# Kernel optimization log

Hardware: AMD Instinct MI355X
Metric: run time of the kernel (lower is better)

## Reference

```python
import jax, jax.numpy as jnp
import numpy as np

N_NODES = 100000
N_EDGES = 800000
HID = 128
EDIM = 32


def _mlp2(x, W1, b1, W2, b2):
    return jax.nn.relu(x @ W1 + b1) @ W2 + b2


def _edge_conv(x, src, dst, edge_attr, We1, be1, We2, be2, Wm1, bm1, Wm2, bm2):
    # edge-conditioned message: msg_mlp(x_j + edge_proj(edge_attr)), scatter-add to dst
    e = _mlp2(edge_attr, We1, be1, We2, be2)          # [E, HID]
    m = _mlp2(x[src] + e, Wm1, bm1, Wm2, bm2)          # [E, HID]
    return jax.ops.segment_sum(m, dst, num_segments=x.shape[0])


def setup_inputs() -> dict:
    key = jax.random.key(0)
    ks = jax.random.split(key, 12)
    s = 0.05
    inp = {
        "x": jax.random.normal(ks[0], (N_NODES, HID), dtype=jnp.float32),
        "edge_index": jax.random.randint(ks[1], (2, N_EDGES), 0, N_NODES, dtype=jnp.int32).astype(jnp.int64),
        "edge_attr": jax.random.normal(ks[2], (N_EDGES, EDIM), dtype=jnp.float32),
        "alpha": jnp.zeros((), dtype=jnp.float32),
    }
    i = 3
    for pfx in ("f", "b"):
        inp[f"{pfx}_We1"] = jax.random.normal(ks[i], (EDIM, HID), dtype=jnp.float32) * s; i += 1
        inp[f"{pfx}_be1"] = jnp.zeros((HID,), dtype=jnp.float32)
        inp[f"{pfx}_We2"] = jax.random.normal(ks[i], (HID, HID), dtype=jnp.float32) * s; i += 1
        inp[f"{pfx}_be2"] = jnp.zeros((HID,), dtype=jnp.float32)
        inp[f"{pfx}_Wm1"] = jax.random.normal(ks[i], (HID, HID), dtype=jnp.float32) * s; i += 1
        inp[f"{pfx}_bm1"] = jnp.zeros((HID,), dtype=jnp.float32)
        inp[f"{pfx}_Wm2"] = jax.random.normal(ks[i], (HID, HID), dtype=jnp.float32) * s; i += 1
        inp[f"{pfx}_bm2"] = jnp.zeros((HID,), dtype=jnp.float32)
    return inp


def reference(x, edge_index, edge_attr,
              f_We1, f_be1, f_We2, f_be2, f_Wm1, f_bm1, f_Wm2, f_bm2,
              b_We1, b_be1, b_We2, b_be2, b_Wm1, b_bm1, b_Wm2, b_bm2,
              alpha):
    src, dst = edge_index[0], edge_index[1]
    # forward direction: messages from src aggregated at dst (PyG source_to_target)
    h_fwd = _edge_conv(x, src, dst, edge_attr, f_We1, f_be1, f_We2, f_be2,
                       f_Wm1, f_bm1, f_Wm2, f_bm2)
    # backward direction: edge_index flipped
    h_bwd = _edge_conv(x, dst, src, edge_attr, b_We1, b_be1, b_We2, b_be2,
                       b_Wm1, b_bm1, b_Wm2, b_bm2)
    a = jax.nn.sigmoid(alpha)
    return a * h_fwd + (1.0 - a) * h_bwd
```

## Files before the change

kernel.cpp:

```cpp
#include <hip/hip_runtime.h>
#include <hip/hip_bf16.h>

#define E_EDGES   800000
#define N_NODES   100000
#define HIDN      128
#define EDIMN     32
#define TILE      128
#define NT        (E_EDGES / TILE)
#define GRID_MAIN 256
#define STR       35
#define NB_BLK    ((N_NODES + 1023) / 1024)

typedef __attribute__((ext_vector_type(8))) short bf16x8;
typedef __attribute__((ext_vector_type(4))) float f32x4;
typedef __attribute__((ext_vector_type(4))) unsigned int u32x4;

static __device__ __forceinline__ unsigned short f2bf(float f) {
  unsigned int u = __float_as_uint(f);
  u += 0x7fffu + ((u >> 16) & 1u);
  return (unsigned short)(u >> 16);
}
static __device__ __forceinline__ unsigned int pk2f(float a, float b) {
  __hip_bfloat162 h = __float22bfloat162_rn(make_float2(a, b));
  unsigned short lo = __hip_bfloat16_raw(h.x).x;
  unsigned short hi = __hip_bfloat16_raw(h.y).x;
  return (unsigned int)lo | ((unsigned int)hi << 16);
}
static __device__ __forceinline__ int swz(int row, int kElem) {
  return row * HIDN + (kElem ^ ((row & 7) << 3));
}
static __device__ __forceinline__ int swz32(int row, int kElem) {
  return row * EDIMN + (kElem ^ ((row & 3) << 3));
}
static __device__ __forceinline__ int nmap(int k) {
  return ((k >> 5) << 5) | (((k & 7) >> 2) << 4) | (((k >> 3) & 3) << 2) | (k & 3);
}

template <bool RELU>
static __device__ __forceinline__ void packB(const f32x4* acc, bf16x8* B) {
#pragma unroll
  for (int ks = 0; ks < 4; ++ks) {
    f32x4 a = acc[2 * ks], b = acc[2 * ks + 1];
    if (RELU) {
#pragma unroll
      for (int j = 0; j < 4; ++j) { a[j] = fmaxf(a[j], 0.f); b[j] = fmaxf(b[j], 0.f); }
    }
    u32x4 t;
    t[0] = pk2f(a[0], a[1]); t[1] = pk2f(a[2], a[3]);
    t[2] = pk2f(b[0], b[1]); t[3] = pk2f(b[2], b[3]);
    union { u32x4 u; bf16x8 v; } cvt;
    cvt.u = t;
    B[ks] = cvt.v;
  }
}

static __device__ __forceinline__ void mmT(const unsigned short* W, f32x4* a0, f32x4* a1,
                                           const bf16x8* B0, const bf16x8* B1,
                                           int c16, int q) {
#pragma unroll
  for (int cb = 0; cb < 8; ++cb) {
#pragma unroll
    for (int ks = 0; ks < 4; ++ks) {
      bf16x8 w = *reinterpret_cast<const bf16x8*>(&W[swz(cb * 16 + c16, ks * 32 + q * 8)]);
      a0[cb] = __builtin_amdgcn_mfma_f32_16x16x32_bf16(w, B0[ks], a0[cb], 0, 0, 0);
      a1[cb] = __builtin_amdgcn_mfma_f32_16x16x32_bf16(w, B1[ks], a1[cb], 0, 0, 0);
    }
  }
}

__global__ void k_detect(const int* __restrict__ ei, int* __restrict__ flag) {
  __shared__ int nz;
  if (threadIdx.x == 0) nz = 0;
  __syncthreads();
  if (ei[2 * threadIdx.x + 1] != 0) atomicAdd(&nz, 1);
  __syncthreads();
  if (threadIdx.x == 0) flag[0] = (nz == 0) ? 1 : 0;
}

__global__ void k_norm(const int* __restrict__ ei, const int* __restrict__ flag,
                       int* __restrict__ idx) {
  const int stride = gridDim.x * blockDim.x;
  const int w = flag[0];
  for (int i = blockIdx.x * blockDim.x + threadIdx.x; i < 2 * E_EDGES; i += stride)
    idx[i] = w ? ei[2 * i] : ei[i];
}

__global__ void k_hist(const int* __restrict__ srcI, const int* __restrict__ dstI,
                       int* __restrict__ histD, int* __restrict__ histS) {
  const int stride = gridDim.x * blockDim.x;
  for (int e = blockIdx.x * blockDim.x + threadIdx.x; e < E_EDGES; e += stride) {
    atomicAdd(&histD[dstI[e]], 1);
    atomicAdd(&histS[srcI[e]], 1);
  }
}

__global__ void k_scan1(const int* __restrict__ in, int* __restrict__ out,
                        int* __restrict__ part, int n) {
  __shared__ int buf[1024];
  const int t = threadIdx.x;
  const int i = blockIdx.x * 1024 + t;
  int v = (i < n) ? in[i] : 0;
  buf[t] = v;
  __syncthreads();
  int acc = v;
  for (int off = 1; off < 1024; off <<= 1) {
    int add = (t >= off) ? buf[t - off] : 0;
    __syncthreads();
    acc += add;
    buf[t] = acc;
    __syncthreads();
  }
  if (i < n) out[i] = acc - v;
  if (t == 1023) part[blockIdx.x] = acc;
}

__global__ void k_scan2(int* __restrict__ partD, int* __restrict__ partS, int nb) {
  if (threadIdx.x == 0) {
    int s = 0;
    for (int i = 0; i < nb; ++i) { int v = partD[i]; partD[i] = s; s += v; }
  }
  if (threadIdx.x == 1) {
    int s = 0;
    for (int i = 0; i < nb; ++i) { int v = partS[i]; partS[i] = s; s += v; }
  }
}

__global__ void k_scan3(int* __restrict__ base, int* __restrict__ cur,
                        const int* __restrict__ part, int n) {
  const int i = blockIdx.x * 1024 + threadIdx.x;
  if (i < n) {
    int b = base[i] + part[blockIdx.x];
    base[i] = b;
    cur[i] = b;
  }
}

__global__ void k_place(const int* __restrict__ srcI, const int* __restrict__ dstI,
                        int* __restrict__ curD, int* __restrict__ curS,
                        int* __restrict__ eF, int* __restrict__ gF, int* __restrict__ sF,
                        int* __restrict__ eB, int* __restrict__ gB, int* __restrict__ sB) {
  const int stride = gridDim.x * blockDim.x;
  for (int e = blockIdx.x * blockDim.x + threadIdx.x; e < E_EDGES; e += stride) {
    const int s = srcI[e], d = dstI[e];
    int p = atomicAdd(&curD[d], 1);
    eF[p] = e; gF[p] = s; sF[p] = d;
    int p2 = atomicAdd(&curS[s], 1);
    eB[p2] = e; gB[p2] = d; sB[p2] = s;
  }
}

__launch_bounds__(256, 1)
__global__ void k_conv(const float* __restrict__ x, const float* __restrict__ ea,
                       const int* __restrict__ eidx,
                       const int* __restrict__ gidx, const int* __restrict__ sidx,
                       const float* __restrict__ We1, const float* __restrict__ be1,
                       const float* __restrict__ We2, const float* __restrict__ be2,
                       const float* __restrict__ Wm1, const float* __restrict__ bm1,
                       const float* __restrict__ Wm2, const float* __restrict__ bm2,
                       const float* __restrict__ alphap, int dir,
                       float* __restrict__ out) {
  __shared__ unsigned short wt[3][HIDN * HIDN];
  __shared__ unsigned short w1[HIDN * EDIMN];
  __shared__ float stg[4][32][STR];
  __shared__ float b1l[HIDN];
  __shared__ float b3l[HIDN];
  __shared__ float b4l[HIDN];

  const int tid = threadIdx.x;
  const int wv  = tid >> 6;
  const int ln  = tid & 63;
  const int q   = ln >> 4;
  const int c16 = ln & 15;

  const float sg    = 1.f / (1.f + expf(-alphap[0]));
  const float scale = dir ? (1.f - sg) : sg;

  {
    const float* Ws[3] = {We2, Wm1, Wm2};
    for (int m = 0; m < 3; ++m) {
      const float s = (m == 2) ? scale : 1.f;
      const float* W = Ws[m];
      for (int p = tid; p < HIDN * HIDN; p += 256) {
        int n = p & (HIDN - 1), k = p >> 7;
        wt[m][swz(n, k)] = f2bf(W[nmap(k) * HIDN + n] * s);
      }
    }
    for (int p = tid; p < HIDN * EDIMN; p += 256) {
      int n = p & (HIDN - 1), k = p >> 7;
      w1[swz32(n, k)] = f2bf(We1[k * HIDN + n]);
    }
    for (int n = tid; n < HIDN; n += 256) {
      b1l[n] = be1[n];
      b4l[n] = bm2[n] * scale;
      float acc = bm1[n];
      for (int k = 0; k < HIDN; ++k) acc += be2[k] * Wm1[k * HIDN + n];
      b3l[n] = acc;
    }
  }
  __syncthreads();

  const int o4 = q * 4;
  const bool sorted = (eidx != nullptr);

  for (int t = blockIdx.x; t < NT; t += GRID_MAIN) {
    const int e0w = t * TILE + wv * 32;
    const int e_  = e0w + c16;

    const int ee0 = sorted ? eidx[e_] : e_;
    const int ee1 = sorted ? eidx[e_ + 16] : (e_ + 16);
    f32x4 e0a = *reinterpret_cast<const f32x4*>(&ea[(size_t)ee0 * EDIMN + q * 8]);
    f32x4 e0b = *reinterpret_cast<const f32x4*>(&ea[(size_t)ee0 * EDIMN + q * 8 + 4]);
    f32x4 e1a = *reinterpret_cast<const f32x4*>(&ea[(size_t)ee1 * EDIMN + q * 8]);
    f32x4 e1b = *reinterpret_cast<const f32x4*>(&ea[(size_t)ee1 * EDIMN + q * 8 + 4]);
    const int gi0 = gidx[e_], gi1 = gidx[e_ + 16];

    const int rowK = sidx[e0w + (ln & 31)];
    const int rowN = sidx[e0w + (ln & 31) + ((ln & 31) < 31 ? 1 : 0)];
    const unsigned long long mask =
        __ballot((ln < 31) && (rowK == rowN));

    int sirC[2][4];
#pragma unroll
    for (int mb = 0; mb < 2; ++mb)
#pragma unroll
      for (int j = 0; j < 4; ++j)
        sirC[mb][j] = sidx[e0w + 16 * mb + 4 * q + j];

    int rend[2][4];
#pragma unroll
    for (int mb = 0; mb < 2; ++mb)
#pragma unroll
      for (int j = 0; j < 4; ++j) {
        const int r = 16 * mb + 4 * q + j;
        const bool head = (r == 0) || !((mask >> (r - 1)) & 1ull);
        int e = r;
        if (head)
          e = r + 1 + (int)__builtin_ctzll(~(mask >> r));
        rend[mb][j] = e;
      }

    f32x4 A0[8], A1[8];
    bf16x8 B0[4], B1[4];

    {
      u32x4 t0, t1;
      t0[0] = pk2f(e0a[0], e0a[1]); t0[1] = pk2f(e0a[2], e0a[3]);
      t0[2] = pk2f(e0b[0], e0b[1]); t0[3] = pk2f(e0b[2], e0b[3]);
      t1[0] = pk2f(e1a[0], e1a[1]); t1[1] = pk2f(e1a[2], e1a[3]);
      t1[2] = pk2f(e1b[0], e1b[1]); t1[3] = pk2f(e1b[2], e1b[3]);
      union { u32x4 u; bf16x8 v; } c0, c1;
      c0.u = t0; c1.u = t1;
      bf16x8 E0 = c0.v;
      bf16x8 E1 = c1.v;
#pragma unroll
      for (int cb = 0; cb < 8; ++cb) {
        A0[cb] = *reinterpret_cast<const f32x4*>(&b1l[cb * 16 + o4]);
        A1[cb] = A0[cb];
      }
#pragma unroll
      for (int cb = 0; cb < 8; ++cb) {
        bf16x8 w = *reinterpret_cast<const bf16x8*>(&w1[swz32(cb * 16 + c16, q * 8)]);
        A0[cb] = __builtin_amdgcn_mfma_f32_16x16x32_bf16(w, E0, A0[cb], 0, 0, 0);
        A1[cb] = __builtin_amdgcn_mfma_f32_16x16x32_bf16(w, E1, A1[cb], 0, 0, 0);
      }
      packB<true>(A0, B0);
      packB<true>(A1, B1);
    }

#pragma unroll
    for (int cb = 0; cb < 8; ++cb) {
      A0[cb] = *reinterpret_cast<const f32x4*>(&x[(size_t)gi0 * HIDN + cb * 16 + o4]);
      A1[cb] = *reinterpret_cast<const f32x4*>(&x[(size_t)gi1 * HIDN + cb * 16 + o4]);
    }
    mmT(&wt[0][0], A0, A1, B0, B1, c16, q);
    packB<false>(A0, B0);
    packB<false>(A1, B1);

#pragma unroll
    for (int cb = 0; cb < 8; ++cb) {
      A0[cb] = *reinterpret_cast<const f32x4*>(&b3l[cb * 16 + o4]);
      A1[cb] = A0[cb];
    }
    mmT(&wt[1][0], A0, A1, B0, B1, c16, q);
    packB<true>(A0, B0);
    packB<true>(A1, B1);

#pragma unroll
    for (int cb = 0; cb < 8; ++cb) {
      A0[cb] = *reinterpret_cast<const f32x4*>(&b4l[cb * 16 + o4]);
      A1[cb] = A0[cb];
    }
    mmT(&wt[2][0], A0, A1, B0, B1, c16, q);

#pragma unroll
    for (int p = 0; p < 4; ++p) {
#pragma unroll
      for (int cb2 = 0; cb2 < 2; ++cb2) {
        const int cb = 2 * p + cb2;
#pragma unroll
        for (int j = 0; j < 4; ++j) {
          stg[wv][c16][16 * cb2 + q + 4 * j]      = A0[cb][j];
          stg[wv][c16 + 16][16 * cb2 + q + 4 * j] = A1[cb][j];
        }
      }
      const int ca = c16 >> 2, cbt = c16 & 3;
#pragma unroll
      for (int mb = 0; mb < 2; ++mb)
#pragma unroll
        for (int j = 0; j < 4; ++j) {
          const int r  = 16 * mb + 4 * q + j;
          const int re = rend[mb][j];
          if (re > r) {
            float acc0 = 0.f, acc1 = 0.f;
            for (int rr = r; rr < re; ++rr) {
              acc0 += stg[wv][rr][4 * cbt + ca];
              acc1 += stg[wv][rr][16 + 4 * cbt + ca];
            }
            float* po = out + (size_t)sirC[mb][j] * HIDN + 32 * p + c16;
            unsafeAtomicAdd(po, acc0);
            unsafeAtomicAdd(po + 16, acc1);
          }
        }
    }
  }
}

extern "C" void kernel_launch(void* const* d_in, const int* in_sizes, int n_in,
                              void* d_out, int out_size, void* d_ws, size_t ws_size,
                              hipStream_t stream) {
  const float* x     = (const float*)d_in[0];
  const int*   ei    = (const int*)d_in[1];
  const float* ea    = (const float*)d_in[2];
  const float* alpha = (const float*)d_in[3];
  const float* fWe1 = (const float*)d_in[4],  *fbe1 = (const float*)d_in[5];
  const float* fWe2 = (const float*)d_in[6],  *fbe2 = (const float*)d_in[7];
  const float* fWm1 = (const float*)d_in[8],  *fbm1 = (const float*)d_in[9];
  const float* fWm2 = (const float*)d_in[10], *fbm2 = (const float*)d_in[11];
  const float* bWe1 = (const float*)d_in[12], *bbe1 = (const float*)d_in[13];
  const float* bWe2 = (const float*)d_in[14], *bbe2 = (const float*)d_in[15];
  const float* bWm1 = (const float*)d_in[16], *bbm1 = (const float*)d_in[17];
  const float* bWm2 = (const float*)d_in[18], *bbm2 = (const float*)d_in[19];
  float* out = (float*)d_out;

  char* w = (char*)d_ws;
  int* flag = (int*)w;

  const size_t BINS = 400000;
  const size_t EB   = (size_t)E_EDGES * 4;
  const size_t need = 256 + 4 * BINS + 1024 + 8 * EB;
  const bool doSort = (ws_size >= need);

  hipMemsetAsync(d_out, 0, (size_t)out_size * sizeof(float), stream);
  k_detect<<<1, 256, 0, stream>>>(ei, flag);

  if (doSort) {
    size_t off = 256;
    int* histD = (int*)(w + off); off += BINS;
    int* histS = (int*)(w + off); off += BINS;
    int* baseD = (int*)(w + off); off += BINS;
    int* baseS = (int*)(w + off); off += BINS;
    int* partD = (int*)(w + off); off += 512;
    int* partS = (int*)(w + off); off += 512;
    int* srcI  = (int*)(w + off); off += EB;
    int* dstI  = (int*)(w + off); off += EB;
    int* eF    = (int*)(w + off); off += EB;
    int* gF    = (int*)(w + off); off += EB;
    int* sF    = (int*)(w + off); off += EB;
    int* eB2   = (int*)(w + off); off += EB;
    int* gB2   = (int*)(w + off); off += EB;
    int* sB2   = (int*)(w + off); off += EB;
    int* idx   = srcI;

    k_norm<<<2048, 256, 0, stream>>>(ei, flag, idx);
    hipMemsetAsync(histD, 0, 2 * BINS, stream);
    k_hist<<<2048, 256, 0, stream>>>(srcI, dstI, histD, histS);
    k_scan1<<<NB_BLK, 1024, 0, stream>>>(histD, baseD, partD, N_NODES);
    k_scan1<<<NB_BLK, 1024, 0, stream>>>(histS, baseS, partS, N_NODES);
    k_scan2<<<1, 64, 0, stream>>>(partD, partS, NB_BLK);
    k_scan3<<<NB_BLK, 1024, 0, stream>>>(baseD, histD, partD, N_NODES);
    k_scan3<<<NB_BLK, 1024, 0, stream>>>(baseS, histS, partS, N_NODES);
    k_place<<<2048, 256, 0, stream>>>(srcI, dstI, histD, histS,
                                      eF, gF, sF, eB2, gB2, sB2);

    k_conv<<<GRID_MAIN, 256, 0, stream>>>(x, ea, eF, gF, sF,
                                          fWe1, fbe1, fWe2, fbe2, fWm1, fbm1, fWm2, fbm2,
                                          alpha, 0, out);
    k_conv<<<GRID_MAIN, 256, 0, stream>>>(x, ea, eB2, gB2, sB2,
                                          bWe1, bbe1, bWe2, bbe2, bWm1, bbm1, bWm2, bbm2,
                                          alpha, 1, out);
  } else {
    int* idx  = (int*)(w + 256);
    int* srcI = idx;
    int* dstI = idx + E_EDGES;
    k_norm<<<2048, 256, 0, stream>>>(ei, flag, idx);
    k_conv<<<GRID_MAIN, 256, 0, stream>>>(x, ea, nullptr, srcI, dstI,
                                          fWe1, fbe1, fWe2, fbe2, fWm1, fbm1, fWm2, fbm2,
                                          alpha, 0, out);
    k_conv<<<GRID_MAIN, 256, 0, stream>>>(x, ea, nullptr, dstI, srcI,
                                          bWe1, bbe1, bWe2, bbe2, bWm1, bbm1, bWm2, bbm2,
                                          alpha, 1, out);
  }
}
```

Baseline: 947.3 us.

## Replace serial per-lane segment reduction with shuffle segmented scan and head-row atomics

Each lane used to walk its own run of equal-destination rows in the staging tile, sum them serially and issue its own atomics. Now every lane loads a row slice as float4 vectors and runs a log-step shuffle-based segmented reduction bounded by each run's end. Head rows write their sums back to LDS, and then a loop over head rows issues coalesced 32-lane atomics per destination row. The goal is fewer serialized LDS reads and more coalesced atomics, at the cost of many cross-lane shuffles per pass and possibly misaligned vector LDS accesses on the padded row stride.

```diff
diff --git a/kernel.cpp b/kernel.cpp
--- a/kernel.cpp
+++ b/kernel.cpp
@@ -216,28 +216,7 @@
 
     const int rowK = sidx[e0w + (ln & 31)];
     const int rowN = sidx[e0w + (ln & 31) + ((ln & 31) < 31 ? 1 : 0)];
-    const unsigned long long mask =
-        __ballot((ln < 31) && (rowK == rowN));
-
-    int sirC[2][4];
-#pragma unroll
-    for (int mb = 0; mb < 2; ++mb)
-#pragma unroll
-      for (int j = 0; j < 4; ++j)
-        sirC[mb][j] = sidx[e0w + 16 * mb + 4 * q + j];
-
-    int rend[2][4];
-#pragma unroll
-    for (int mb = 0; mb < 2; ++mb)
-#pragma unroll
-      for (int j = 0; j < 4; ++j) {
-        const int r = 16 * mb + 4 * q + j;
-        const bool head = (r == 0) || !((mask >> (r - 1)) & 1ull);
-        int e = r;
-        if (head)
-          e = r + 1 + (int)__builtin_ctzll(~(mask >> r));
-        rend[mb][j] = e;
-      }
+    const unsigned long long mask = __ballot((ln < 31) && (rowK == rowN));
 
     f32x4 A0[8], A1[8];
     bf16x8 B0[4], B1[4];
@@ -292,6 +271,12 @@
     }
     mmT(&wt[2][0], A0, A1, B0, B1, c16, q);
 
+    const int r  = ln & 31;
+    const int pl = ln >> 5;
+    const int rend_r = r + 1 + (int)__builtin_ctzll(~(mask >> r));
+    const bool headL = (r == 0) || !((mask >> (r - 1)) & 1ull);
+    const unsigned long long headBits = (~(mask << 1)) & 0xFFFFFFFFull;
+
 #pragma unroll
     for (int p = 0; p < 4; ++p) {
 #pragma unroll
@@ -303,24 +288,46 @@
           stg[wv][c16 + 16][16 * cb2 + q + 4 * j] = A1[cb][j];
         }
       }
-      const int ca = c16 >> 2, cbt = c16 & 3;
-#pragma unroll
-      for (int mb = 0; mb < 2; ++mb)
-#pragma unroll
-        for (int j = 0; j < 4; ++j) {
-          const int r  = 16 * mb + 4 * q + j;
-          const int re = rend[mb][j];
-          if (re > r) {
-            float acc0 = 0.f, acc1 = 0.f;
-            for (int rr = r; rr < re; ++rr) {
-              acc0 += stg[wv][rr][4 * cbt + ca];
-              acc1 += stg[wv][rr][16 + 4 * cbt + ca];
-            }
-            float* po = out + (size_t)sirC[mb][j] * HIDN + 32 * p + c16;
-            unsafeAtomicAdd(po, acc0);
-            unsafeAtomicAdd(po + 16, acc1);
+      f32x4 v0 = *reinterpret_cast<const f32x4*>(&stg[wv][r][pl * 16 + 0]);
+      f32x4 v1 = *reinterpret_cast<const f32x4*>(&stg[wv][r][pl * 16 + 4]);
+      f32x4 v2 = *reinterpret_cast<const f32x4*>(&stg[wv][r][pl * 16 + 8]);
+      f32x4 v3 = *reinterpret_cast<const f32x4*>(&stg[wv][r][pl * 16 + 12]);
+#pragma unroll
+      for (int d = 1; d < 32; d <<= 1) {
+        const int src = (ln & 32) | ((r + d) & 31);
+        f32x4 t0, t1, t2, t3;
+#pragma unroll
+        for (int u = 0; u < 4; ++u) {
+          t0[u] = __shfl(v0[u], src);
+          t1[u] = __shfl(v1[u], src);
+          t2[u] = __shfl(v2[u], src);
+          t3[u] = __shfl(v3[u], src);
+        }
+        if (r + d < rend_r) {
+#pragma unroll
+          for (int u = 0; u < 4; ++u) {
+            v0[u] += t0[u]; v1[u] += t1[u]; v2[u] += t2[u]; v3[u] += t3[u];
           }
         }
+      }
+      if (headL) {
+        *reinterpret_cast<f32x4*>(&stg[wv][r][pl * 16 + 0])  = v0;
+        *reinterpret_cast<f32x4*>(&stg[wv][r][pl * 16 + 4])  = v1;
+        *reinterpret_cast<f32x4*>(&stg[wv][r][pl * 16 + 8])  = v2;
+        *reinterpret_cast<f32x4*>(&stg[wv][r][pl * 16 + 12]) = v3;
+      }
+      unsigned long long hh = headBits;
+      while (hh) {
+        const int rr = (int)__builtin_ctzll(hh);
+        hh &= hh - 1;
+        const int key = __shfl(rowK, rr);
+        if (ln < 32) {
+          const float val = stg[wv][rr][ln];
+          const int m = ln & 15;
+          const int f = 32 * p + 16 * (ln >> 4) + 4 * (m & 3) + (m >> 2);
+          unsafeAtomicAdd(&out[(size_t)key * HIDN + f], val);
+        }
+      }
     }
   }
 }
```

After: 998.0 us. 1.05x slower.
